# Optimization experiments

Hardware: AMD Instinct MI355X
Metric: run time of the kernel (lower is better)

Reference implementation:

```python
import jax, jax.numpy as jnp
import numpy as np


def sparsemax(z):
    # sparsemax along the last axis (matches tfa.activations.sparsemax default axis=-1)
    K = z.shape[-1]
    zs = -jnp.sort(-z, axis=-1)                      # descending sort
    cs = jnp.cumsum(zs, axis=-1)
    k = jnp.arange(1, K + 1, dtype=z.dtype)
    support = 1.0 + k * zs > cs                      # support set indicator
    kmax = jnp.sum(support, axis=-1, keepdims=True)  # |support|, int
    cs_k = jnp.take_along_axis(cs, kmax - 1, axis=-1)
    tau = (cs_k - 1.0) / kmax.astype(z.dtype)
    return jnp.maximum(z - tau, 0.0)


def binary_lut(depth):
    # (depth, 2**depth, 2) table mapping leaf index -> per-level bit / complement
    idx = np.arange(2 ** depth)
    off = 2 ** np.arange(depth)
    bits = (idx[None, :] // off[:, None]) % 2        # (depth, 2**depth)
    return jnp.asarray(np.stack([bits, 1 - bits], axis=-1), dtype=jnp.float32)


def setup_inputs() -> dict:
    key = jax.random.key(0)
    ks = jax.random.split(key, 5)
    B, F, N, D, U = 8192, 256, 128, 6, 16
    return {
        "x": jax.random.normal(ks[0], (B, F), dtype=jnp.float32),
        "feature_selection_logits": jax.random.normal(ks[1], (F, N, D), dtype=jnp.float32),
        "feature_thresholds": jax.random.normal(ks[2], (N, D), dtype=jnp.float32),
        "log_temperatures": jax.random.normal(ks[3], (N, D), dtype=jnp.float32) * 0.1,
        "response": jax.random.normal(ks[4], (N, U, 2 ** D), dtype=jnp.float32),
        "depth": D,
    }


def reference(x, feature_selection_logits, feature_thresholds, log_temperatures, response, depth):
    lut = binary_lut(depth)                                          # (d, 2**d, 2)
    selectors = sparsemax(feature_selection_logits)                  # (i, n, d)
    fv = jnp.einsum('bi,ind->bnd', x, selectors)                     # (b, n, d)
    tl = (fv - feature_thresholds) * jnp.exp(-log_temperatures)      # (b, n, d)
    tl = jnp.stack([-tl, tl], axis=-1)                               # (b, n, d, 2)
    gates = jnp.clip(0.5 * tl + 0.5, 0.0, 1.0)                       # sparsemoid
    rg = jnp.einsum('bnds,dcs->bndc', gates, lut)                    # (b, n, d, 2**d)
    rg = jnp.prod(rg, axis=-2)                                       # (b, n, 2**d)
    resp = jnp.einsum('bnc,nuc->bnu', rg, response)                  # (b, n, u)
    return jnp.mean(resp, axis=1)                                    # (b, u)
```

## Files before the change

### kernel.cpp

```cpp
#include <hip/hip_runtime.h>


typedef float f32x4 __attribute__((ext_vector_type(4)));
typedef unsigned int u32;
typedef _Float16 h16;
typedef _Float16 h16x2 __attribute__((ext_vector_type(2)));
typedef _Float16 h16x8 __attribute__((ext_vector_type(8)));

typedef unsigned short __attribute__((may_alias)) u16a;
typedef u32            __attribute__((may_alias)) u32a;
typedef float          __attribute__((may_alias)) f32a;

#define WPF_OFF   0
#define RESPF_OFF 393216
#define BIAS_OFF  655360

union h2u { h16x2 h; u32 u; };
union hbits { h16 h; unsigned short s; };
union fragh { u32 w[4]; h16x8 v; int4 i4; h16x2 h2[4]; };

__device__ inline unsigned short h16r(float f) {
    hbits t; t.h = (h16)f; return t.s;
}
__device__ inline u32 packh2(float a, float b) {
    h2u t; t.h[0] = (h16)a; t.h[1] = (h16)b; return t.u;
}

__device__ inline f32x4 mfma_f16(h16x8 a, h16x8 b, f32x4 c) {
    return __builtin_amdgcn_mfma_f32_16x16x32_f16(a, b, c, 0, 0, 0);
}

__global__ __launch_bounds__(256) void k_prep(const float* __restrict__ fsl,
                                              const float* __restrict__ thr,
                                              const float* __restrict__ logt,
                                              const float* __restrict__ resp,
                                              unsigned short* __restrict__ WpF,
                                              unsigned short* __restrict__ respF,
                                              float* __restrict__ bias) {
    int bb  = blockIdx.x;
    int tid = threadIdx.x;
    if (bb < 128) {
        __shared__ unsigned short sm[8][192];
        int ib = (bb & 31) * 8;
        int nb = (bb >> 5) * 32;
        int il = tid >> 5;
        int nl = tid & 31;
        int i = ib + il;
        int n = nb + nl;
        const float* zp = fsl + (i * 128 + n) * 6;

        float z[6], zs[6];
        #pragma unroll
        for (int d = 0; d < 6; ++d) { z[d] = zp[d]; zs[d] = z[d]; }
        #pragma unroll
        for (int a = 0; a < 5; ++a) {
            #pragma unroll
            for (int b = a + 1; b < 6; ++b) {
                float hi = fmaxf(zs[a], zs[b]);
                float lo = fminf(zs[a], zs[b]);
                zs[a] = hi; zs[b] = lo;
            }
        }
        float cs = 0.f, csel = 0.f;
        int   km = 1;
        #pragma unroll
        for (int k = 0; k < 6; ++k) {
            cs += zs[k];
            if (1.0f + (float)(k + 1) * zs[k] > cs) { km = k + 1; csel = cs; }
        }
        float tau = (csel - 1.0f) / (float)km;

        #pragma unroll
        for (int d = 0; d < 6; ++d) {
            float invT = expf(-logt[n * 6 + d]);
            float sel  = fmaxf(z[d] - tau, 0.0f);
            float wv   = sel * 0.5f * invT;
            sm[il][nl * 6 + d] = h16r(wv);
            if (i == 0) bias[n * 6 + d] = 0.5f - 0.5f * invT * thr[n * 6 + d];
        }
        __syncthreads();

        if (tid < 192) {
            int ct  = (nb * 6) / 16 + (tid >> 4);
            int clm = tid & 15;
            int kt  = ib >> 5;
            int lq  = (ib >> 3) & 3;
            union { unsigned short s[8]; int4 i4; } o;
            #pragma unroll
            for (int j = 0; j < 8; ++j) o.s[j] = sm[j][tid];
            *(int4*)(WpF + (size_t)(((ct * 8 + kt) * 64 + lq * 16 + clm) * 8)) = o.i4;
        }
    } else {
        int t = (bb - 128) * 256 + tid;
        int n  = t >> 7;
        int k2 = (t >> 6) & 1;
        int l  = t & 63;
        int u  = l & 15;
        int c0 = k2 * 32 + (l >> 4) * 8;
        const float* rp = resp + n * 1024 + u * 64 + c0;
        float4 ra = *(const float4*)rp;
        float4 rb = *(const float4*)(rp + 4);
        int4 o;
        o.x = (int)packh2(ra.x, ra.y);
        o.y = (int)packh2(ra.z, ra.w);
        o.z = (int)packh2(rb.x, rb.y);
        o.w = (int)packh2(rb.z, rb.w);
        ((int4*)respF)[(n * 2 + k2) * 64 + l] = o;
    }
}

__global__ __launch_bounds__(1024, 4) void k_main(const float* __restrict__ x,
                                                  const unsigned short* __restrict__ WpF,
                                                  const unsigned short* __restrict__ respF,
                                                  const float* __restrict__ bias,
                                                  float* __restrict__ out) {
    __shared__ char smemraw[65536];
    const int4* xf4 = (const int4*)smemraw;

    int tid = threadIdx.x;
    int w  = tid >> 6;
    int l  = tid & 63;
    int cl = l & 15;
    int lq = l >> 4;
    int rowbase = blockIdx.x * 32;
    int ctbase  = w * 3;

    u16a* gw = (u16a*)(smemraw + 16384 + w * 3072);
    const int4* wp4 = (const int4*)WpF;
    const int4* rp4 = (const int4*)respF;

    {
        int k8  = tid & 31;
        int row = tid >> 5;
        const float* xp = x + (size_t)(rowbase + row) * 256 + k8 * 8;
        float4 xa = *(const float4*)(xp);
        float4 xb = *(const float4*)(xp + 4);
        int4 p;
        p.x = (int)packh2(xa.x, xa.y);
        p.y = (int)packh2(xa.z, xa.w);
        p.z = (int)packh2(xb.x, xb.y);
        p.w = (int)packh2(xb.z, xb.w);
        int rt = row >> 4, rl = row & 15, kt = k8 >> 2, klq = k8 & 3;
        char* basep = smemraw + (size_t)(rt * 8 + kt) * 1024
                              + (size_t)(((klq * 16 + rl) ^ kt) * 16);
        *(int4*)basep = p;
    }

    fragh bc[3];
    #pragma unroll
    for (int j = 0; j < 3; ++j)
        bc[j].i4 = wp4[((ctbase + j) * 8 + 0) * 64 + l];

    __syncthreads();

    f32x4 acc[3][2];
    #pragma unroll
    for (int j = 0; j < 3; ++j) {
        acc[j][0] = (f32x4){0.f, 0.f, 0.f, 0.f};
        acc[j][1] = (f32x4){0.f, 0.f, 0.f, 0.f};
    }

    #pragma unroll
    for (int kt = 0; kt < 8; ++kt) {
        fragh bn[3];
        if (kt < 7) {
            #pragma unroll
            for (int j = 0; j < 3; ++j)
                bn[j].i4 = wp4[((ctbase + j) * 8 + kt + 1) * 64 + l];
        }
        fragh ah0, ah1;
        ah0.i4 = xf4[(0 * 8 + kt) * 64 + (l ^ kt)];
        ah1.i4 = xf4[(1 * 8 + kt) * 64 + (l ^ kt)];
        #pragma unroll
        for (int j = 0; j < 3; ++j)
            acc[j][0] = mfma_f16(ah0.v, bc[j].v, acc[j][0]);
        #pragma unroll
        for (int j = 0; j < 3; ++j)
            acc[j][1] = mfma_f16(ah1.v, bc[j].v, acc[j][1]);
        if (kt < 7) {
            bc[0] = bn[0]; bc[1] = bn[1]; bc[2] = bn[2];
        }
    }

    fragh rc0, rc1;
    rc0.i4 = rp4[((w * 8 + 0) * 2 + 0) * 64 + l];
    rc1.i4 = rp4[((w * 8 + 0) * 2 + 1) * 64 + l];

    #pragma unroll
    for (int j = 0; j < 3; ++j) {
        int colg = (ctbase + j) * 16 + cl;
        int coll = j * 16 + cl;
        float bv = bias[colg];
        #pragma unroll
        for (int rt = 0; rt < 2; ++rt) {
            #pragma unroll
            for (int r = 0; r < 4; ++r) {
                float g = acc[j][rt][r] + bv;
                g = fminf(fmaxf(g, 0.f), 1.f);
                int row = rt * 16 + lq * 4 + r;
                gw[row * 48 + coll] = h16r(g);
            }
        }
    }

    f32x4 oacc0 = (f32x4){0.f, 0.f, 0.f, 0.f};
    f32x4 oacc1 = (f32x4){0.f, 0.f, 0.f, 0.f};
    const h16x2 onev = (h16x2){(h16)1.0f, (h16)1.0f};

    #pragma unroll
    for (int t2 = 0; t2 < 8; ++t2) {
        fragh rn0, rn1;
        if (t2 < 7) {
            rn0.i4 = rp4[((w * 8 + t2 + 1) * 2 + 0) * 64 + l];
            rn1.i4 = rp4[((w * 8 + t2 + 1) * 2 + 1) * 64 + l];
        }
        #pragma unroll
        for (int rt = 0; rt < 2; ++rt) {
            int row = rt * 16 + cl;
            const u32a* gp = (const u32a*)((const char*)gw + row * 96 + t2 * 12);
            h2u g01u, g23u, g45u;
            g01u.u = gp[0]; g23u.u = gp[1]; g45u.u = gp[2];
            h16x2 g01 = g01u.h, g23 = g23u.h, g45 = g45u.h;
            h16x2 s01 = onev - g01;
            h16x2 s23 = onev - g23;
            h16x2 s45 = onev - g45;
            h16x2 gs0  = __builtin_shufflevector(g01, s01, 0, 2);
            h16x2 b1g  = __builtin_shufflevector(g01, g01, 1, 1);
            h16x2 b1s  = __builtin_shufflevector(s01, s01, 1, 1);
            h16x2 t01a = gs0 * b1g;
            h16x2 t01b = gs0 * b1s;
            h16x2 g2b  = __builtin_shufflevector(g23, g23, 0, 0);
            h16x2 s2b  = __builtin_shufflevector(s23, s23, 0, 0);
            h16x2 pa01 = t01a * g2b;
            h16x2 pa23 = t01b * g2b;
            h16x2 pa45 = t01a * s2b;
            h16x2 pa67 = t01b * s2b;
            h16 f3  = (lq & 1) ? s23[1] : g23[1];
            h16 f4  = (lq & 2) ? s45[0] : g45[0];
            h16 m34 = f3 * f4;
            h16 pbl = m34 * g45[1];
            h16 pbh = m34 * s45[1];
            h16x2 pblb = (h16x2){pbl, pbl};
            h16x2 pbhb = (h16x2){pbh, pbh};
            fragh fa1, fa2;
            fa1.h2[0] = pa01 * pblb; fa1.h2[1] = pa23 * pblb;
            fa1.h2[2] = pa45 * pblb; fa1.h2[3] = pa67 * pblb;
            fa2.h2[0] = pa01 * pbhb; fa2.h2[1] = pa23 * pbhb;
            fa2.h2[2] = pa45 * pbhb; fa2.h2[3] = pa67 * pbhb;
            if (rt == 0) {
                oacc0 = mfma_f16(fa1.v, rc0.v, oacc0);
                oacc0 = mfma_f16(fa2.v, rc1.v, oacc0);
            } else {
                oacc1 = mfma_f16(fa1.v, rc0.v, oacc1);
                oacc1 = mfma_f16(fa2.v, rc1.v, oacc1);
            }
        }
        if (t2 < 7) { rc0 = rn0; rc1 = rn1; }
    }

    {
        f32a* pw = (f32a*)(smemraw + 16384 + w * 3072);
        int us = (cl + w) & 15;
        #pragma unroll
        for (int r = 0; r < 4; ++r) {
            pw[(lq * 4 + r) * 16 + us]        = oacc0[r];
            pw[(16 + lq * 4 + r) * 16 + us]   = oacc1[r];
        }
    }
    __syncthreads();

    if (tid < 512) {
        int r = tid >> 4, u = tid & 15;
        const f32a* pb = (const f32a*)(smemraw + 16384);
        float s = 0.f;
        #pragma unroll
        for (int ww = 0; ww < 16; ++ww)
            s += pb[ww * 768 + r * 16 + ((u + ww) & 15)];
        out[(size_t)(rowbase + r) * 16 + u] = s * (1.0f / 128.0f);
    }
}

extern "C" void kernel_launch(void* const* d_in, const int* in_sizes, int n_in,
                              void* d_out, int out_size, void* d_ws, size_t ws_size,
                              hipStream_t stream) {
    (void)in_sizes; (void)n_in; (void)out_size; (void)ws_size;
    const float* x    = (const float*)d_in[0];
    const float* fsl  = (const float*)d_in[1];
    const float* thr  = (const float*)d_in[2];
    const float* logt = (const float*)d_in[3];
    const float* resp = (const float*)d_in[4];

    char* ws = (char*)d_ws;
    unsigned short* WpF   = (unsigned short*)(ws + WPF_OFF);
    unsigned short* respF = (unsigned short*)(ws + RESPF_OFF);
    float*          bias  = (float*)(ws + BIAS_OFF);
    float* out = (float*)d_out;

    k_prep<<<192, 256, 0, stream>>>(fsl, thr, logt, resp, WpF, respF, bias);
    k_main<<<256, 1024, 0, stream>>>(x, WpF, respF, bias, out);
}
```

Measured before the change: 21.03 us.

## Split trees across two blocks per row tile and combine partials in new kernel

The main kernel now launches 512 blocks of 512 threads, each covering half of the 128 trees for a 32-row tile, instead of 256 blocks of 1024 threads covering all trees. Each block writes its partial sums to workspace, and a new combine kernel adds the two halves and applies the mean scaling. The aim is more blocks to fill the device and smaller blocks that need less shared memory. In exchange, each x tile is loaded and converted twice, partials make an extra round trip through global memory, and a third kernel launch adds overhead.

```diff
diff --git a/kernel.cpp b/kernel.cpp
--- a/kernel.cpp
+++ b/kernel.cpp
@@ -14,6 +14,7 @@
 #define WPF_OFF   0
 #define RESPF_OFF 393216
 #define BIAS_OFF  655360
+#define PART_OFF  658432
 
 union h2u { h16x2 h; u32 u; };
 union hbits { h16 h; unsigned short s; };
@@ -109,12 +110,12 @@
     }
 }
 
-__global__ __launch_bounds__(1024, 4) void k_main(const float* __restrict__ x,
-                                                  const unsigned short* __restrict__ WpF,
-                                                  const unsigned short* __restrict__ respF,
-                                                  const float* __restrict__ bias,
-                                                  float* __restrict__ out) {
-    __shared__ char smemraw[65536];
+__global__ __launch_bounds__(512, 4) void k_main(const float* __restrict__ x,
+                                                 const unsigned short* __restrict__ WpF,
+                                                 const unsigned short* __restrict__ respF,
+                                                 const float* __restrict__ bias,
+                                                 float* __restrict__ part) {
+    __shared__ char smemraw[40960];
     const int4* xf4 = (const int4*)smemraw;
 
     int tid = threadIdx.x;
@@ -122,16 +123,20 @@
     int l  = tid & 63;
     int cl = l & 15;
     int lq = l >> 4;
-    int rowbase = blockIdx.x * 32;
-    int ctbase  = w * 3;
+    int th = blockIdx.x & 1;
+    int rowbase = (blockIdx.x >> 1) * 32;
+    int ctbase  = th * 24 + w * 3;
+    int ntree   = th * 64 + w * 8;
 
     u16a* gw = (u16a*)(smemraw + 16384 + w * 3072);
     const int4* wp4 = (const int4*)WpF;
     const int4* rp4 = (const int4*)respF;
 
-    {
-        int k8  = tid & 31;
-        int row = tid >> 5;
+    #pragma unroll
+    for (int it = 0; it < 2; ++it) {
+        int a   = it * 512 + tid;
+        int k8  = a & 31;
+        int row = a >> 5;
         const float* xp = x + (size_t)(rowbase + row) * 256 + k8 * 8;
         float4 xa = *(const float4*)(xp);
         float4 xb = *(const float4*)(xp + 4);
@@ -183,8 +188,8 @@
     }
 
     fragh rc0, rc1;
-    rc0.i4 = rp4[((w * 8 + 0) * 2 + 0) * 64 + l];
-    rc1.i4 = rp4[((w * 8 + 0) * 2 + 1) * 64 + l];
+    rc0.i4 = rp4[((ntree + 0) * 2 + 0) * 64 + l];
+    rc1.i4 = rp4[((ntree + 0) * 2 + 1) * 64 + l];
 
     #pragma unroll
     for (int j = 0; j < 3; ++j) {
@@ -211,8 +216,8 @@
     for (int t2 = 0; t2 < 8; ++t2) {
         fragh rn0, rn1;
         if (t2 < 7) {
-            rn0.i4 = rp4[((w * 8 + t2 + 1) * 2 + 0) * 64 + l];
-            rn1.i4 = rp4[((w * 8 + t2 + 1) * 2 + 1) * 64 + l];
+            rn0.i4 = rp4[((ntree + t2 + 1) * 2 + 0) * 64 + l];
+            rn1.i4 = rp4[((ntree + t2 + 1) * 2 + 1) * 64 + l];
         }
         #pragma unroll
         for (int rt = 0; rt < 2; ++rt) {
@@ -269,15 +274,24 @@
     }
     __syncthreads();
 
-    if (tid < 512) {
+    {
         int r = tid >> 4, u = tid & 15;
         const f32a* pb = (const f32a*)(smemraw + 16384);
         float s = 0.f;
         #pragma unroll
-        for (int ww = 0; ww < 16; ++ww)
+        for (int ww = 0; ww < 8; ++ww)
             s += pb[ww * 768 + r * 16 + ((u + ww) & 15)];
-        out[(size_t)(rowbase + r) * 16 + u] = s * (1.0f / 128.0f);
-    }
+        part[(size_t)blockIdx.x * 512 + tid] = s;
+    }
+}
+
+__global__ __launch_bounds__(512) void k_comb(const float* __restrict__ part,
+                                              float* __restrict__ out) {
+    int b = blockIdx.x;
+    int tid = threadIdx.x;
+    size_t o = (size_t)b * 512 + tid;
+    float v = part[(size_t)(2 * b) * 512 + tid] + part[(size_t)(2 * b + 1) * 512 + tid];
+    out[o] = v * (1.0f / 128.0f);
 }
 
 extern "C" void kernel_launch(void* const* d_in, const int* in_sizes, int n_in,
@@ -294,8 +308,10 @@
     unsigned short* WpF   = (unsigned short*)(ws + WPF_OFF);
     unsigned short* respF = (unsigned short*)(ws + RESPF_OFF);
     float*          bias  = (float*)(ws + BIAS_OFF);
+    float*          part  = (float*)(ws + PART_OFF);
     float* out = (float*)d_out;
 
     k_prep<<<192, 256, 0, stream>>>(fsl, thr, logt, resp, WpF, respF, bias);
-    k_main<<<256, 1024, 0, stream>>>(x, WpF, respF, bias, out);
-}
+    k_main<<<512, 512, 0, stream>>>(x, WpF, respF, bias, part);
+    k_comb<<<256, 512, 0, stream>>>(part, out);
+}
```

Result: slower. 21.57 us (+2.6%).

## Prefetch weight and response fragments deeper into registers with compiler fences

Applied to the files above, without the earlier changes.

The weight fragments for two column tiles are loaded fully into registers before the barrier. The third tile's fragments are streamed in during the first MMA pass, and the GEMM loop is restructured per column tile. Response fragments are prefetched four steps ahead instead of one, and empty asm memory fences pin the load placement. This aims to hide global load latency behind MFMA work, at the cost of much higher VGPR usage, which could reduce occupancy or cause spills.

```diff
diff --git a/kernel.cpp b/kernel.cpp
--- a/kernel.cpp
+++ b/kernel.cpp
@@ -10,6 +10,8 @@
 typedef unsigned short __attribute__((may_alias)) u16a;
 typedef u32            __attribute__((may_alias)) u32a;
 typedef float          __attribute__((may_alias)) f32a;
+
+#define MEMFENCE asm volatile("" ::: "memory")
 
 #define WPF_OFF   0
 #define RESPF_OFF 393216
@@ -146,10 +148,14 @@
         *(int4*)basep = p;
     }
 
-    fragh bc[3];
-    #pragma unroll
-    for (int j = 0; j < 3; ++j)
-        bc[j].i4 = wp4[((ctbase + j) * 8 + 0) * 64 + l];
+    fragh B0[8], B1[8], B2[8];
+    #pragma unroll
+    for (int kt = 0; kt < 8; ++kt)
+        B0[kt].i4 = wp4[((ctbase + 0) * 8 + kt) * 64 + l];
+    #pragma unroll
+    for (int kt = 0; kt < 8; ++kt)
+        B1[kt].i4 = wp4[((ctbase + 1) * 8 + kt) * 64 + l];
+    MEMFENCE;
 
     __syncthreads();
 
@@ -162,29 +168,38 @@
 
     #pragma unroll
     for (int kt = 0; kt < 8; ++kt) {
-        fragh bn[3];
-        if (kt < 7) {
-            #pragma unroll
-            for (int j = 0; j < 3; ++j)
-                bn[j].i4 = wp4[((ctbase + j) * 8 + kt + 1) * 64 + l];
-        }
-        fragh ah0, ah1;
-        ah0.i4 = xf4[(0 * 8 + kt) * 64 + (l ^ kt)];
-        ah1.i4 = xf4[(1 * 8 + kt) * 64 + (l ^ kt)];
-        #pragma unroll
-        for (int j = 0; j < 3; ++j)
-            acc[j][0] = mfma_f16(ah0.v, bc[j].v, acc[j][0]);
-        #pragma unroll
-        for (int j = 0; j < 3; ++j)
-            acc[j][1] = mfma_f16(ah1.v, bc[j].v, acc[j][1]);
-        if (kt < 7) {
-            bc[0] = bn[0]; bc[1] = bn[1]; bc[2] = bn[2];
-        }
-    }
-
-    fragh rc0, rc1;
-    rc0.i4 = rp4[((w * 8 + 0) * 2 + 0) * 64 + l];
-    rc1.i4 = rp4[((w * 8 + 0) * 2 + 1) * 64 + l];
+        B2[kt].i4 = wp4[((ctbase + 2) * 8 + kt) * 64 + l];
+        fragh a0, a1;
+        a0.i4 = xf4[(0 * 8 + kt) * 64 + (l ^ kt)];
+        a1.i4 = xf4[(1 * 8 + kt) * 64 + (l ^ kt)];
+        acc[0][0] = mfma_f16(a0.v, B0[kt].v, acc[0][0]);
+        acc[0][1] = mfma_f16(a1.v, B0[kt].v, acc[0][1]);
+        MEMFENCE;
+    }
+    #pragma unroll
+    for (int kt = 0; kt < 8; ++kt) {
+        fragh a0, a1;
+        a0.i4 = xf4[(0 * 8 + kt) * 64 + (l ^ kt)];
+        a1.i4 = xf4[(1 * 8 + kt) * 64 + (l ^ kt)];
+        acc[1][0] = mfma_f16(a0.v, B1[kt].v, acc[1][0]);
+        acc[1][1] = mfma_f16(a1.v, B1[kt].v, acc[1][1]);
+    }
+    #pragma unroll
+    for (int kt = 0; kt < 8; ++kt) {
+        fragh a0, a1;
+        a0.i4 = xf4[(0 * 8 + kt) * 64 + (l ^ kt)];
+        a1.i4 = xf4[(1 * 8 + kt) * 64 + (l ^ kt)];
+        acc[2][0] = mfma_f16(a0.v, B2[kt].v, acc[2][0]);
+        acc[2][1] = mfma_f16(a1.v, B2[kt].v, acc[2][1]);
+    }
+
+    fragh R[8][2];
+    #pragma unroll
+    for (int t2 = 0; t2 < 4; ++t2) {
+        R[t2][0].i4 = rp4[((w * 8 + t2) * 2 + 0) * 64 + l];
+        R[t2][1].i4 = rp4[((w * 8 + t2) * 2 + 1) * 64 + l];
+    }
+    MEMFENCE;
 
     #pragma unroll
     for (int j = 0; j < 3; ++j) {
@@ -209,10 +224,10 @@
 
     #pragma unroll
     for (int t2 = 0; t2 < 8; ++t2) {
-        fragh rn0, rn1;
-        if (t2 < 7) {
-            rn0.i4 = rp4[((w * 8 + t2 + 1) * 2 + 0) * 64 + l];
-            rn1.i4 = rp4[((w * 8 + t2 + 1) * 2 + 1) * 64 + l];
+        if (t2 < 4) {
+            R[t2 + 4][0].i4 = rp4[((w * 8 + t2 + 4) * 2 + 0) * 64 + l];
+            R[t2 + 4][1].i4 = rp4[((w * 8 + t2 + 4) * 2 + 1) * 64 + l];
+            MEMFENCE;
         }
         #pragma unroll
         for (int rt = 0; rt < 2; ++rt) {
@@ -248,14 +263,13 @@
             fa2.h2[0] = pa01 * pbhb; fa2.h2[1] = pa23 * pbhb;
             fa2.h2[2] = pa45 * pbhb; fa2.h2[3] = pa67 * pbhb;
             if (rt == 0) {
-                oacc0 = mfma_f16(fa1.v, rc0.v, oacc0);
-                oacc0 = mfma_f16(fa2.v, rc1.v, oacc0);
+                oacc0 = mfma_f16(fa1.v, R[t2][0].v, oacc0);
+                oacc0 = mfma_f16(fa2.v, R[t2][1].v, oacc0);
             } else {
-                oacc1 = mfma_f16(fa1.v, rc0.v, oacc1);
-                oacc1 = mfma_f16(fa2.v, rc1.v, oacc1);
+                oacc1 = mfma_f16(fa1.v, R[t2][0].v, oacc1);
+                oacc1 = mfma_f16(fa2.v, R[t2][1].v, oacc1);
             }
         }
-        if (t2 < 7) { rc0 = rn0; rc1 = rn1; }
     }
 
     {
```

Measured after the change: 20.90 us. Within noise of the previous version (-0.6%).
